# Kernel optimization log

Hardware: AMD Instinct MI355X
Metric: run time of the kernel (lower is better)

## Reference

```python
import jax, jax.numpy as jnp
import numpy as np
from jax.scipy.special import gammaln

N_NODES = 50000
N_EDGES = 1600000
IN_DIM, H1, H2 = 512, 256, 129  # H2 = hid_dims[-1] + 1 (kappa column)


def setup_inputs() -> dict:
    key = jax.random.key(0)
    k1, k2, k3, k4 = jax.random.split(key, 4)
    x = jax.random.normal(k1, (N_NODES, IN_DIM), dtype=jnp.float32)
    edge_index = jax.random.randint(k2, (2, N_EDGES), 0, N_NODES, dtype=jnp.int32)
    # Glorot-ish init for GCN weights
    W0 = jax.random.normal(k3, (IN_DIM, H1), dtype=jnp.float32) * (1.0 / np.sqrt(IN_DIM))
    W1 = jax.random.normal(k4, (H1, H2), dtype=jnp.float32) * (1.0 / np.sqrt(H1))
    return {"x": x, "edge_index": edge_index, "W0": W0, "W1": W1}


def _gcn_conv(h, W, src, dst, norm, n):
    # PyG GCNConv (bias=False): h' = D^-1/2 (A+I) D^-1/2 (h W)
    h = h @ W
    msg = h[src] * norm[:, None]          # [E+N, F_out]
    return jax.ops.segment_sum(msg, dst, num_segments=n)


def reference(x, edge_index, W0, W1):
    n = x.shape[0]
    loops = jnp.arange(n, dtype=edge_index.dtype)
    src = jnp.concatenate([edge_index[0], loops])
    dst = jnp.concatenate([edge_index[1], loops])
    # symmetric normalization with self-loops (deg >= 1, so rsqrt is safe)
    deg = jax.ops.segment_sum(jnp.ones_like(dst, dtype=x.dtype), dst, num_segments=n)
    dinv = jax.lax.rsqrt(deg)
    norm = dinv[src] * dinv[dst]          # [E+N]

    h = jax.nn.softplus(_gcn_conv(x, W0, src, dst, norm, n))
    # dropout is identity in eval mode (training=False)
    h = jax.nn.softplus(_gcn_conv(h, W1, src, dst, norm, n))

    lbd = h[:, :-1]                       # [N, 128] Weibull scale
    kappa = h[:, -1:] + 0.1               # [N, 1]   Weibull shape
    # deterministic (non-random-encoder / eval) reparameterization:
    # z = lbd * exp(lgamma(1 + 1/kappa))  == E[Weibull(lbd, kappa)]
    z = lbd * jnp.exp(gammaln(1.0 + 1.0 / kappa))
    return z, lbd, kappa
```

## Files before the change

kernel.cpp:

```cpp
#include <hip/hip_runtime.h>
#include <hip/hip_bf16.h>
#include <math.h>


typedef unsigned short ushort_t;
typedef __attribute__((ext_vector_type(8))) short bf16x8;
typedef __attribute__((ext_vector_type(4))) float f32x4;

__device__ __forceinline__ ushort_t f2bf(float f) {
    union { float f; unsigned u; } x; x.f = f;
    unsigned r = x.u + 0x7FFF + ((x.u >> 16) & 1);
    return (ushort_t)(r >> 16);
}
__device__ __forceinline__ float bf2f(ushort_t s) {
    union { unsigned u; float f; } x; x.u = ((unsigned)s) << 16; return x.f;
}

__device__ __forceinline__ void async_copy16(const void* gsrc, void* ldst) {
    __builtin_amdgcn_global_load_lds(
        (const __attribute__((address_space(1))) unsigned int*)gsrc,
        (__attribute__((address_space(3))) unsigned int*)ldst,
        16, 0, 0);
}


__global__ __launch_bounds__(256) void count_kernel(const int* __restrict__ dst,
                                                    int* __restrict__ cnt, int E)
{
    int e = blockIdx.x * blockDim.x + threadIdx.x;
    if (e < E) atomicAdd(&cnt[dst[e]], 1);
}

__global__ __launch_bounds__(1024) void scan_local(const int* __restrict__ cnt,
                                                   int* __restrict__ rowptr,
                                                   float* __restrict__ dinv,
                                                   int* __restrict__ blksum, int N)
{
    __shared__ int wsum[16];
    int tid = threadIdx.x, lane = tid & 63, wid = tid >> 6;
    int i = blockIdx.x * 1024 + tid;
    int v = (i < N) ? cnt[i] : 0;
    if (i < N) dinv[i] = rsqrtf((float)(v + 1));
    int s = v;
#pragma unroll
    for (int off = 1; off < 64; off <<= 1) {
        int t = __shfl_up(s, off, 64);
        if (lane >= off) s += t;
    }
    if (lane == 63) wsum[wid] = s;
    __syncthreads();
    if (tid < 16) {
        int w = wsum[tid];
#pragma unroll
        for (int off = 1; off < 16; off <<= 1) {
            int t = __shfl_up(w, off, 64);
            if (tid >= off) w += t;
        }
        wsum[tid] = w;
    }
    __syncthreads();
    int excl = s - v + (wid ? wsum[wid - 1] : 0);
    if (i < N) rowptr[i] = excl;
    if (tid == 0) blksum[blockIdx.x] = wsum[15];
}

__global__ __launch_bounds__(64) void scan_blk(const int* __restrict__ blksum,
                                               int* __restrict__ blkoff,
                                               int nblk, int* __restrict__ rowptr, int N)
{
    int tid = threadIdx.x;
    int v = (tid < nblk) ? blksum[tid] : 0;
    int s = v;
#pragma unroll
    for (int off = 1; off < 64; off <<= 1) {
        int t = __shfl_up(s, off, 64);
        if (tid >= off) s += t;
    }
    if (tid < nblk) blkoff[tid] = s - v;
    if (tid == nblk - 1) rowptr[N] = s;
}

__global__ __launch_bounds__(256) void scan_add(int* __restrict__ rowptr,
                                                int* __restrict__ cursor,
                                                const int* __restrict__ blkoff, int N)
{
    int i = blockIdx.x * blockDim.x + threadIdx.x;
    if (i < N) {
        int r = rowptr[i] + blkoff[i >> 10];
        rowptr[i] = r;
        cursor[i] = r;
    }
}

__global__ __launch_bounds__(256) void scatter_kernel(const int* __restrict__ src,
                                                      const int* __restrict__ dst,
                                                      int* __restrict__ cursor,
                                                      int* __restrict__ col, int E)
{
    int e = blockIdx.x * blockDim.x + threadIdx.x;
    if (e < E) {
        int d = dst[e];
        int pos = atomicAdd(&cursor[d], 1);
        col[pos] = src[e];
    }
}


__global__ __launch_bounds__(256) void conv_x(const float* __restrict__ x,
                                              ushort_t* __restrict__ Abig,
                                              int M, int M_pad)
{
    int id = blockIdx.x * blockDim.x + threadIdx.x;
    int r = id >> 7, q = id & 127;
    if (r >= M_pad) return;
    float4 v = make_float4(0.f, 0.f, 0.f, 0.f);
    if (r < M) v = *reinterpret_cast<const float4*>(&x[(size_t)r * 512 + q * 4]);
    ushort4 h, l;
    h.x = f2bf(v.x); l.x = f2bf(v.x - bf2f(h.x));
    h.y = f2bf(v.y); l.y = f2bf(v.y - bf2f(h.y));
    h.z = f2bf(v.z); l.z = f2bf(v.z - bf2f(h.z));
    h.w = f2bf(v.w); l.w = f2bf(v.w - bf2f(h.w));
    ushort_t* rowp = Abig + (size_t)r * 1024;
    *reinterpret_cast<ushort4*>(rowp + q * 4)       = h;
    *reinterpret_cast<ushort4*>(rowp + 512 + q * 4) = l;
}

__global__ __launch_bounds__(256) void conv_w0(const float* __restrict__ W0,
                                               ushort_t* __restrict__ BT)
{
    int id = blockIdx.x * blockDim.x + threadIdx.x;
    int k = id & 511, n = id >> 9;
    if (n >= 256) return;
    float v = W0[(size_t)k * 256 + n];
    ushort_t h = f2bf(v);
    ushort_t l = f2bf(v - bf2f(h));
    ushort_t* rowp = BT + (size_t)n * 1536;
    rowp[k] = h; rowp[512 + k] = h; rowp[1024 + k] = l;
}

__global__ __launch_bounds__(256) void conv_w1(const float* __restrict__ W1,
                                               ushort_t* __restrict__ BT,
                                               float* __restrict__ W1col)
{
    int id = blockIdx.x * blockDim.x + threadIdx.x;
    int k = id & 255, n = id >> 8;
    if (n >= 128) return;
    float v = W1[(size_t)k * 129 + n];
    ushort_t h = f2bf(v);
    ushort_t l = f2bf(v - bf2f(h));
    ushort_t* rowp = BT + (size_t)n * 768;
    rowp[k] = h; rowp[256 + k] = h; rowp[512 + k] = l;
    if (n == 0) W1col[k] = W1[(size_t)k * 129 + 128];
}

__global__ __launch_bounds__(256) void gemm_bf16(const ushort_t* __restrict__ A, int lda,
                                                 const ushort_t* __restrict__ BT, int ldbt,
                                                 float* __restrict__ C, int ldc,
                                                 int M, int K, int kwrap)
{
    __shared__ short As[128 * 32];
    __shared__ short Bs[128 * 32];

    int tid  = threadIdx.x;
    int w    = tid >> 6;
    int lane = tid & 63;
    int lm   = lane & 15;
    int lq   = lane >> 4;
    int bm   = blockIdx.x * 128;
    int bn   = blockIdx.y * 128;
    int wr   = (w >> 1) * 64;
    int wc   = (w & 1) * 64;

    f32x4 acc[4][4];
#pragma unroll
    for (int i = 0; i < 4; ++i)
#pragma unroll
        for (int j = 0; j < 4; ++j) acc[i][j] = (f32x4)(0.f);

    int srow = (lane >> 2);
    int scol = (lane & 3) * 16;

    for (int k0 = 0; k0 < K; k0 += 32) {
        int ka = (k0 < kwrap) ? k0 : (k0 - kwrap);
#pragma unroll
        for (int q = 0; q < 2; ++q) {
            int r = w * 32 + q * 16 + srow;
            const char* ga = (const char*)A + ((size_t)(bm + r) * lda + ka) * 2 + scol;
            async_copy16(ga, (char*)As + (size_t)(w * 32 + q * 16) * 64);
        }
#pragma unroll
        for (int q = 0; q < 2; ++q) {
            int r = w * 32 + q * 16 + srow;
            const char* gb = (const char*)BT + ((size_t)(bn + r) * ldbt + k0) * 2 + scol;
            async_copy16(gb, (char*)Bs + (size_t)(w * 32 + q * 16) * 64);
        }
        __syncthreads();

        bf16x8 afr[4], bfr[4];
#pragma unroll
        for (int mi = 0; mi < 4; ++mi)
            afr[mi] = *reinterpret_cast<const bf16x8*>(&As[(wr + mi * 16 + lm) * 32 + lq * 8]);
#pragma unroll
        for (int ni = 0; ni < 4; ++ni)
            bfr[ni] = *reinterpret_cast<const bf16x8*>(&Bs[(wc + ni * 16 + lm) * 32 + lq * 8]);
#pragma unroll
        for (int mi = 0; mi < 4; ++mi)
#pragma unroll
            for (int ni = 0; ni < 4; ++ni)
                acc[mi][ni] = __builtin_amdgcn_mfma_f32_16x16x32_bf16(
                    afr[mi], bfr[ni], acc[mi][ni], 0, 0, 0);
        __syncthreads();
    }

#pragma unroll
    for (int mi = 0; mi < 4; ++mi) {
#pragma unroll
        for (int ni = 0; ni < 4; ++ni) {
            int rbase = bm + wr + mi * 16 + lq * 4;
            int cc    = bn + wc + ni * 16 + lm;
#pragma unroll
            for (int e = 0; e < 4; ++e) {
                int r = rbase + e;
                if (r < M) C[(size_t)r * ldc + cc] = acc[mi][ni][e];
            }
        }
    }
}


__device__ __forceinline__ float softplus_f(float x)
{
    return fmaxf(x, 0.f) + log1pf(expf(-fabsf(x)));
}

__device__ __forceinline__ void fma4(float4& a, float w, const float4& v)
{
    a.x = fmaf(w, v.x, a.x);
    a.y = fmaf(w, v.y, a.y);
    a.z = fmaf(w, v.z, a.z);
    a.w = fmaf(w, v.w, a.w);
}

__global__ __launch_bounds__(256) void agg1_kernel(const float* __restrict__ T1,
                                                   const float* __restrict__ dinv,
                                                   const int* __restrict__ rowptr,
                                                   const int* __restrict__ col,
                                                   ushort_t* __restrict__ H1big, int N)
{
    int node = blockIdx.x;
    int tid  = threadIdx.x;
    int c    = tid & 63;
    int slot = tid >> 6;
    float di = dinv[node];
    int beg = rowptr[node], end = rowptr[node + 1];

    float4 acc = make_float4(0.f, 0.f, 0.f, 0.f);
    __shared__ int    s_src[256];
    __shared__ float  s_w[256];
    __shared__ float4 red[4][64];

    for (int base = beg; base < end; base += 256) {
        int cnt = min(256, end - base);
        if (tid < cnt) {
            int s = col[base + tid];
            s_src[tid] = s;
            s_w[tid]   = dinv[s];
        }
        __syncthreads();
        int jb = 0;
        int lim = cnt & ~15;
        for (; jb < lim; jb += 16) {
            int j0 = jb + slot, j1 = j0 + 4, j2 = j0 + 8, j3 = j0 + 12;
            int   s0 = s_src[j0], s1 = s_src[j1], s2 = s_src[j2], s3 = s_src[j3];
            float w0 = s_w[j0],  w1 = s_w[j1],  w2 = s_w[j2],  w3 = s_w[j3];
            float4 v0 = *reinterpret_cast<const float4*>(&T1[(size_t)s0 * 256 + c * 4]);
            float4 v1 = *reinterpret_cast<const float4*>(&T1[(size_t)s1 * 256 + c * 4]);
            float4 v2 = *reinterpret_cast<const float4*>(&T1[(size_t)s2 * 256 + c * 4]);
            float4 v3 = *reinterpret_cast<const float4*>(&T1[(size_t)s3 * 256 + c * 4]);
            fma4(acc, w0, v0); fma4(acc, w1, v1); fma4(acc, w2, v2); fma4(acc, w3, v3);
        }
        for (; jb < cnt; jb += 4) {
            int j = jb + slot;
            if (j < cnt) {
                int   s = s_src[j];
                float w = s_w[j];
                float4 v = *reinterpret_cast<const float4*>(&T1[(size_t)s * 256 + c * 4]);
                fma4(acc, w, v);
            }
        }
        __syncthreads();
    }

    red[slot][c] = acc;
    __syncthreads();
    if (slot == 0) {
        float4 a0 = red[0][c], a1 = red[1][c], a2 = red[2][c], a3 = red[3][c];
        float4 self = *reinterpret_cast<const float4*>(&T1[(size_t)node * 256 + c * 4]);
        float4 o;
        o.x = softplus_f((a0.x + a1.x + a2.x + a3.x + self.x * di) * di);
        o.y = softplus_f((a0.y + a1.y + a2.y + a3.y + self.y * di) * di);
        o.z = softplus_f((a0.z + a1.z + a2.z + a3.z + self.z * di) * di);
        o.w = softplus_f((a0.w + a1.w + a2.w + a3.w + self.w * di) * di);
        ushort4 h, l;
        h.x = f2bf(o.x); l.x = f2bf(o.x - bf2f(h.x));
        h.y = f2bf(o.y); l.y = f2bf(o.y - bf2f(h.y));
        h.z = f2bf(o.z); l.z = f2bf(o.z - bf2f(h.z));
        h.w = f2bf(o.w); l.w = f2bf(o.w - bf2f(h.w));
        ushort_t* rowp = H1big + (size_t)node * 512;
        *reinterpret_cast<ushort4*>(rowp + c * 4)       = h;
        *reinterpret_cast<ushort4*>(rowp + 256 + c * 4) = l;
    }
}

__global__ __launch_bounds__(256) void kappa_col_kernel(const ushort_t* __restrict__ H1big,
                                                        const float* __restrict__ W1col,
                                                        float* __restrict__ T2k, int N)
{
    __shared__ float w[256];
    int tid = threadIdx.x;
    w[tid] = W1col[tid];
    __syncthreads();
    int lane = tid & 63;
    int wid  = tid >> 6;
    int row  = blockIdx.x * 4 + wid;
    if (row >= N) return;
    const ushort_t* rowp = H1big + (size_t)row * 512;
    float s = 0.f;
#pragma unroll
    for (int k = lane; k < 256; k += 64) {
        float hv = bf2f(rowp[k]) + bf2f(rowp[256 + k]);
        s = fmaf(hv, w[k], s);
    }
#pragma unroll
    for (int off = 32; off > 0; off >>= 1)
        s += __shfl_down(s, off, 64);
    if (lane == 0) T2k[row] = s;
}

__global__ __launch_bounds__(256) void agg2_kernel(const float* __restrict__ T2,
                                                   const float* __restrict__ T2k,
                                                   const float* __restrict__ dinv,
                                                   const int* __restrict__ rowptr,
                                                   const int* __restrict__ col,
                                                   float* __restrict__ z_out,
                                                   float* __restrict__ lbd_out,
                                                   float* __restrict__ kap_out, int N)
{
    int node = blockIdx.x;
    int tid  = threadIdx.x;
    int c    = tid & 31;
    int slot = tid >> 5;
    float di = dinv[node];
    int beg = rowptr[node], end = rowptr[node + 1];

    float4 acc  = make_float4(0.f, 0.f, 0.f, 0.f);
    float  acck = 0.f;
    __shared__ int    s_src[256];
    __shared__ float  s_w[256];
    __shared__ float4 red[8][32];
    __shared__ float  s_kred[4];
    __shared__ float  s_g;

    for (int base = beg; base < end; base += 256) {
        int cnt = min(256, end - base);
        if (tid < cnt) {
            int s = col[base + tid];
            float w = dinv[s];
            s_src[tid] = s;
            s_w[tid]   = w;
            acck = fmaf(w, T2k[s], acck);
        }
        __syncthreads();
        int jb = 0;
        int lim = cnt & ~31;
        for (; jb < lim; jb += 32) {
            int j0 = jb + slot, j1 = j0 + 8, j2 = j0 + 16, j3 = j0 + 24;
            int   s0 = s_src[j0], s1 = s_src[j1], s2 = s_src[j2], s3 = s_src[j3];
            float w0 = s_w[j0],  w1 = s_w[j1],  w2 = s_w[j2],  w3 = s_w[j3];
            float4 v0 = *reinterpret_cast<const float4*>(&T2[(size_t)s0 * 128 + c * 4]);
            float4 v1 = *reinterpret_cast<const float4*>(&T2[(size_t)s1 * 128 + c * 4]);
            float4 v2 = *reinterpret_cast<const float4*>(&T2[(size_t)s2 * 128 + c * 4]);
            float4 v3 = *reinterpret_cast<const float4*>(&T2[(size_t)s3 * 128 + c * 4]);
            fma4(acc, w0, v0); fma4(acc, w1, v1); fma4(acc, w2, v2); fma4(acc, w3, v3);
        }
        for (; jb < cnt; jb += 8) {
            int j = jb + slot;
            if (j < cnt) {
                int   s = s_src[j];
                float w = s_w[j];
                float4 v = *reinterpret_cast<const float4*>(&T2[(size_t)s * 128 + c * 4]);
                fma4(acc, w, v);
            }
        }
        __syncthreads();
    }

#pragma unroll
    for (int off = 32; off > 0; off >>= 1)
        acck += __shfl_down(acck, off, 64);
    if ((tid & 63) == 0) s_kred[tid >> 6] = acck;

    red[slot][c] = acc;
    __syncthreads();

    if (tid == 0) {
        float ak = (s_kred[0] + s_kred[1] + s_kred[2] + s_kred[3] + T2k[node] * di) * di;
        float kv = softplus_f(ak) + 0.1f;
        s_g = expf(lgammaf(1.0f + 1.0f / kv));
        kap_out[node] = kv;
    }
    __syncthreads();

    if (slot == 0) {
        float4 a = red[0][c];
#pragma unroll
        for (int p = 1; p < 8; ++p) {
            float4 b = red[p][c];
            a.x += b.x; a.y += b.y; a.z += b.z; a.w += b.w;
        }
        float4 self = *reinterpret_cast<const float4*>(&T2[(size_t)node * 128 + c * 4]);
        float4 sp;
        sp.x = softplus_f((a.x + self.x * di) * di);
        sp.y = softplus_f((a.y + self.y * di) * di);
        sp.z = softplus_f((a.z + self.z * di) * di);
        sp.w = softplus_f((a.w + self.w * di) * di);
        float g = s_g;
        size_t o = (size_t)node * 128 + c * 4;
        *reinterpret_cast<float4*>(&lbd_out[o]) = sp;
        float4 zv = make_float4(sp.x * g, sp.y * g, sp.z * g, sp.w * g);
        *reinterpret_cast<float4*>(&z_out[o]) = zv;
    }
}

extern "C" void kernel_launch(void* const* d_in, const int* in_sizes, int n_in,
                              void* d_out, int out_size, void* d_ws, size_t ws_size,
                              hipStream_t stream)
{
    const float* x  = (const float*)d_in[0];
    const int*   ei = (const int*)d_in[1];
    const float* W0 = (const float*)d_in[2];
    const float* W1 = (const float*)d_in[3];

    const int N = in_sizes[0] / 512;
    const int E = in_sizes[1] / 2;
    const int* src = ei;
    const int* dst = ei + E;

    const int mblocks = (N + 127) / 128;
    const int M_pad   = mblocks * 128;
    const int nchunk  = (N + 1023) / 1024;

    char* w = (char*)d_ws;
    size_t off = 0;
    auto take = [&](size_t bytes) -> void* {
        void* p = (void*)(w + off);
        off = (off + bytes + 255) & ~(size_t)255;
        return p;
    };
    int*      cnt    = (int*)take((size_t)N * 4);
    int*      rowptr = (int*)take((size_t)(N + 1) * 4);
    int*      cursor = (int*)take((size_t)N * 4);
    float*    dinv   = (float*)take((size_t)N * 4);
    int*      col    = (int*)take((size_t)E * 4);
    int*      blksum = (int*)take(64 * 4);
    int*      blkoff = (int*)take(64 * 4);
    ushort_t* W0bigT = (ushort_t*)take((size_t)256 * 1536 * 2);
    ushort_t* W1bigT = (ushort_t*)take((size_t)128 * 768 * 2);
    float*    W1col  = (float*)take((size_t)256 * 4);
    float*    T2k    = (float*)take((size_t)N * 4);
    float*    T1     = (float*)take((size_t)N * 256 * 4);
    float*    T2     = T1;
    ushort_t* Abig   = (ushort_t*)take((size_t)M_pad * 1024 * 2);
    ushort_t* H1big  = Abig;

    float* z_out   = (float*)d_out;
    float* lbd_out = z_out + (size_t)N * 128;
    float* kap_out = lbd_out + (size_t)N * 128;

    hipMemsetAsync(cnt, 0, (size_t)N * 4, stream);
    count_kernel<<<(E + 255) / 256, 256, 0, stream>>>(dst, cnt, E);
    scan_local<<<nchunk, 1024, 0, stream>>>(cnt, rowptr, dinv, blksum, N);
    scan_blk<<<1, 64, 0, stream>>>(blksum, blkoff, nchunk, rowptr, N);
    scan_add<<<(N + 255) / 256, 256, 0, stream>>>(rowptr, cursor, blkoff, N);
    scatter_kernel<<<(E + 255) / 256, 256, 0, stream>>>(src, dst, cursor, col, E);

    conv_x<<<(M_pad * 128) / 256, 256, 0, stream>>>(x, Abig, N, M_pad);
    conv_w0<<<(256 * 512) / 256, 256, 0, stream>>>(W0, W0bigT);
    conv_w1<<<(128 * 256) / 256, 256, 0, stream>>>(W1, W1bigT, W1col);

    dim3 g1(mblocks, 2);
    gemm_bf16<<<g1, 256, 0, stream>>>(Abig, 1024, W0bigT, 1536, T1, 256, N, 1536, 1024);

    agg1_kernel<<<N, 256, 0, stream>>>(T1, dinv, rowptr, col, H1big, N);

    dim3 g2(mblocks, 1);
    gemm_bf16<<<g2, 256, 0, stream>>>(H1big, 512, W1bigT, 768, T2, 128, N, 768, 512);

    kappa_col_kernel<<<(N + 3) / 4, 256, 0, stream>>>(H1big, W1col, T2k, N);
    agg2_kernel<<<N, 256, 0, stream>>>(T2, T2k, dinv, rowptr, col, z_out, lbd_out, kap_out, N);
}
```

Measured before the change: 840.5 us.

## Aggregate one node per wavefront and fuse kappa column into agg1

Both aggregation kernels now assign a single 64-lane wavefront per node, with four nodes per block, instead of a whole 256-thread block per node. This removes the shared-memory staging, __syncthreads barriers and cross-slot reductions. Each lane keeps four independent accumulators so several neighbour loads stay in flight. The kappa-column dot product is fused into agg1 using the fp32 softplus output, which drops the separate kappa_col kernel and its re-read of H1big. The trade-off is less parallelism per node, since each wave walks the neighbour list serially, and agg2 lanes now issue narrower float2 loads.

```diff
diff --git a/kernel.cpp b/kernel.cpp
--- a/kernel.cpp
+++ b/kernel.cpp
@@ -241,100 +241,68 @@
     a.w = fmaf(w, v.w, a.w);
 }
 
+__device__ __forceinline__ void fma2(float2& a, float w, const float2& v)
+{
+    a.x = fmaf(w, v.x, a.x);
+    a.y = fmaf(w, v.y, a.y);
+}
+
 __global__ __launch_bounds__(256) void agg1_kernel(const float* __restrict__ T1,
                                                    const float* __restrict__ dinv,
                                                    const int* __restrict__ rowptr,
                                                    const int* __restrict__ col,
-                                                   ushort_t* __restrict__ H1big, int N)
-{
-    int node = blockIdx.x;
-    int tid  = threadIdx.x;
-    int c    = tid & 63;
-    int slot = tid >> 6;
+                                                   const float* __restrict__ W1col,
+                                                   ushort_t* __restrict__ H1big,
+                                                   float* __restrict__ T2k, int N)
+{
+    int node = blockIdx.x * 4 + (threadIdx.x >> 6);
+    if (node >= N) return;
+    int lane = threadIdx.x & 63;
     float di = dinv[node];
     int beg = rowptr[node], end = rowptr[node + 1];
 
-    float4 acc = make_float4(0.f, 0.f, 0.f, 0.f);
-    __shared__ int    s_src[256];
-    __shared__ float  s_w[256];
-    __shared__ float4 red[4][64];
-
-    for (int base = beg; base < end; base += 256) {
-        int cnt = min(256, end - base);
-        if (tid < cnt) {
-            int s = col[base + tid];
-            s_src[tid] = s;
-            s_w[tid]   = dinv[s];
-        }
-        __syncthreads();
-        int jb = 0;
-        int lim = cnt & ~15;
-        for (; jb < lim; jb += 16) {
-            int j0 = jb + slot, j1 = j0 + 4, j2 = j0 + 8, j3 = j0 + 12;
-            int   s0 = s_src[j0], s1 = s_src[j1], s2 = s_src[j2], s3 = s_src[j3];
-            float w0 = s_w[j0],  w1 = s_w[j1],  w2 = s_w[j2],  w3 = s_w[j3];
-            float4 v0 = *reinterpret_cast<const float4*>(&T1[(size_t)s0 * 256 + c * 4]);
-            float4 v1 = *reinterpret_cast<const float4*>(&T1[(size_t)s1 * 256 + c * 4]);
-            float4 v2 = *reinterpret_cast<const float4*>(&T1[(size_t)s2 * 256 + c * 4]);
-            float4 v3 = *reinterpret_cast<const float4*>(&T1[(size_t)s3 * 256 + c * 4]);
-            fma4(acc, w0, v0); fma4(acc, w1, v1); fma4(acc, w2, v2); fma4(acc, w3, v3);
-        }
-        for (; jb < cnt; jb += 4) {
-            int j = jb + slot;
-            if (j < cnt) {
-                int   s = s_src[j];
-                float w = s_w[j];
-                float4 v = *reinterpret_cast<const float4*>(&T1[(size_t)s * 256 + c * 4]);
-                fma4(acc, w, v);
-            }
-        }
-        __syncthreads();
-    }
-
-    red[slot][c] = acc;
-    __syncthreads();
-    if (slot == 0) {
-        float4 a0 = red[0][c], a1 = red[1][c], a2 = red[2][c], a3 = red[3][c];
-        float4 self = *reinterpret_cast<const float4*>(&T1[(size_t)node * 256 + c * 4]);
-        float4 o;
-        o.x = softplus_f((a0.x + a1.x + a2.x + a3.x + self.x * di) * di);
-        o.y = softplus_f((a0.y + a1.y + a2.y + a3.y + self.y * di) * di);
-        o.z = softplus_f((a0.z + a1.z + a2.z + a3.z + self.z * di) * di);
-        o.w = softplus_f((a0.w + a1.w + a2.w + a3.w + self.w * di) * di);
-        ushort4 h, l;
-        h.x = f2bf(o.x); l.x = f2bf(o.x - bf2f(h.x));
-        h.y = f2bf(o.y); l.y = f2bf(o.y - bf2f(h.y));
-        h.z = f2bf(o.z); l.z = f2bf(o.z - bf2f(h.z));
-        h.w = f2bf(o.w); l.w = f2bf(o.w - bf2f(h.w));
-        ushort_t* rowp = H1big + (size_t)node * 512;
-        *reinterpret_cast<ushort4*>(rowp + c * 4)       = h;
-        *reinterpret_cast<ushort4*>(rowp + 256 + c * 4) = l;
-    }
-}
-
-__global__ __launch_bounds__(256) void kappa_col_kernel(const ushort_t* __restrict__ H1big,
-                                                        const float* __restrict__ W1col,
-                                                        float* __restrict__ T2k, int N)
-{
-    __shared__ float w[256];
-    int tid = threadIdx.x;
-    w[tid] = W1col[tid];
-    __syncthreads();
-    int lane = tid & 63;
-    int wid  = tid >> 6;
-    int row  = blockIdx.x * 4 + wid;
-    if (row >= N) return;
-    const ushort_t* rowp = H1big + (size_t)row * 512;
-    float s = 0.f;
-#pragma unroll
-    for (int k = lane; k < 256; k += 64) {
-        float hv = bf2f(rowp[k]) + bf2f(rowp[256 + k]);
-        s = fmaf(hv, w[k], s);
-    }
+    float4 a0 = make_float4(0.f, 0.f, 0.f, 0.f);
+    float4 a1 = a0, a2 = a0, a3 = a0;
+
+    int e = beg;
+    for (; e + 4 <= end; e += 4) {
+        int s0 = col[e], s1 = col[e + 1], s2 = col[e + 2], s3 = col[e + 3];
+        float w0 = dinv[s0], w1 = dinv[s1], w2 = dinv[s2], w3 = dinv[s3];
+        float4 v0 = *reinterpret_cast<const float4*>(&T1[(size_t)s0 * 256 + lane * 4]);
+        float4 v1 = *reinterpret_cast<const float4*>(&T1[(size_t)s1 * 256 + lane * 4]);
+        float4 v2 = *reinterpret_cast<const float4*>(&T1[(size_t)s2 * 256 + lane * 4]);
+        float4 v3 = *reinterpret_cast<const float4*>(&T1[(size_t)s3 * 256 + lane * 4]);
+        fma4(a0, w0, v0); fma4(a1, w1, v1); fma4(a2, w2, v2); fma4(a3, w3, v3);
+    }
+    for (; e < end; ++e) {
+        int s = col[e];
+        float w = dinv[s];
+        float4 v = *reinterpret_cast<const float4*>(&T1[(size_t)s * 256 + lane * 4]);
+        fma4(a0, w, v);
+    }
+
+    float4 self = *reinterpret_cast<const float4*>(&T1[(size_t)node * 256 + lane * 4]);
+    float4 o;
+    o.x = softplus_f((a0.x + a1.x + a2.x + a3.x + self.x * di) * di);
+    o.y = softplus_f((a0.y + a1.y + a2.y + a3.y + self.y * di) * di);
+    o.z = softplus_f((a0.z + a1.z + a2.z + a3.z + self.z * di) * di);
+    o.w = softplus_f((a0.w + a1.w + a2.w + a3.w + self.w * di) * di);
+
+    ushort4 h, l;
+    h.x = f2bf(o.x); l.x = f2bf(o.x - bf2f(h.x));
+    h.y = f2bf(o.y); l.y = f2bf(o.y - bf2f(h.y));
+    h.z = f2bf(o.z); l.z = f2bf(o.z - bf2f(h.z));
+    h.w = f2bf(o.w); l.w = f2bf(o.w - bf2f(h.w));
+    ushort_t* rowp = H1big + (size_t)node * 512;
+    *reinterpret_cast<ushort4*>(rowp + lane * 4)       = h;
+    *reinterpret_cast<ushort4*>(rowp + 256 + lane * 4) = l;
+
+    float4 wv = *reinterpret_cast<const float4*>(&W1col[lane * 4]);
+    float tk = o.x * wv.x + o.y * wv.y + o.z * wv.z + o.w * wv.w;
 #pragma unroll
     for (int off = 32; off > 0; off >>= 1)
-        s += __shfl_down(s, off, 64);
-    if (lane == 0) T2k[row] = s;
+        tk += __shfl_down(tk, off, 64);
+    if (lane == 0) T2k[node] = tk;
 }
 
 __global__ __launch_bounds__(256) void agg2_kernel(const float* __restrict__ T2,
@@ -346,90 +314,52 @@
                                                    float* __restrict__ lbd_out,
                                                    float* __restrict__ kap_out, int N)
 {
-    int node = blockIdx.x;
-    int tid  = threadIdx.x;
-    int c    = tid & 31;
-    int slot = tid >> 5;
+    int node = blockIdx.x * 4 + (threadIdx.x >> 6);
+    if (node >= N) return;
+    int lane = threadIdx.x & 63;
     float di = dinv[node];
     int beg = rowptr[node], end = rowptr[node + 1];
 
-    float4 acc  = make_float4(0.f, 0.f, 0.f, 0.f);
-    float  acck = 0.f;
-    __shared__ int    s_src[256];
-    __shared__ float  s_w[256];
-    __shared__ float4 red[8][32];
-    __shared__ float  s_kred[4];
-    __shared__ float  s_g;
-
-    for (int base = beg; base < end; base += 256) {
-        int cnt = min(256, end - base);
-        if (tid < cnt) {
-            int s = col[base + tid];
-            float w = dinv[s];
-            s_src[tid] = s;
-            s_w[tid]   = w;
-            acck = fmaf(w, T2k[s], acck);
-        }
-        __syncthreads();
-        int jb = 0;
-        int lim = cnt & ~31;
-        for (; jb < lim; jb += 32) {
-            int j0 = jb + slot, j1 = j0 + 8, j2 = j0 + 16, j3 = j0 + 24;
-            int   s0 = s_src[j0], s1 = s_src[j1], s2 = s_src[j2], s3 = s_src[j3];
-            float w0 = s_w[j0],  w1 = s_w[j1],  w2 = s_w[j2],  w3 = s_w[j3];
-            float4 v0 = *reinterpret_cast<const float4*>(&T2[(size_t)s0 * 128 + c * 4]);
-            float4 v1 = *reinterpret_cast<const float4*>(&T2[(size_t)s1 * 128 + c * 4]);
-            float4 v2 = *reinterpret_cast<const float4*>(&T2[(size_t)s2 * 128 + c * 4]);
-            float4 v3 = *reinterpret_cast<const float4*>(&T2[(size_t)s3 * 128 + c * 4]);
-            fma4(acc, w0, v0); fma4(acc, w1, v1); fma4(acc, w2, v2); fma4(acc, w3, v3);
-        }
-        for (; jb < cnt; jb += 8) {
-            int j = jb + slot;
-            if (j < cnt) {
-                int   s = s_src[j];
-                float w = s_w[j];
-                float4 v = *reinterpret_cast<const float4*>(&T2[(size_t)s * 128 + c * 4]);
-                fma4(acc, w, v);
-            }
-        }
-        __syncthreads();
-    }
-
-#pragma unroll
-    for (int off = 32; off > 0; off >>= 1)
-        acck += __shfl_down(acck, off, 64);
-    if ((tid & 63) == 0) s_kred[tid >> 6] = acck;
-
-    red[slot][c] = acc;
-    __syncthreads();
-
-    if (tid == 0) {
-        float ak = (s_kred[0] + s_kred[1] + s_kred[2] + s_kred[3] + T2k[node] * di) * di;
-        float kv = softplus_f(ak) + 0.1f;
-        s_g = expf(lgammaf(1.0f + 1.0f / kv));
-        kap_out[node] = kv;
-    }
-    __syncthreads();
-
-    if (slot == 0) {
-        float4 a = red[0][c];
-#pragma unroll
-        for (int p = 1; p < 8; ++p) {
-            float4 b = red[p][c];
-            a.x += b.x; a.y += b.y; a.z += b.z; a.w += b.w;
-        }
-        float4 self = *reinterpret_cast<const float4*>(&T2[(size_t)node * 128 + c * 4]);
-        float4 sp;
-        sp.x = softplus_f((a.x + self.x * di) * di);
-        sp.y = softplus_f((a.y + self.y * di) * di);
-        sp.z = softplus_f((a.z + self.z * di) * di);
-        sp.w = softplus_f((a.w + self.w * di) * di);
-        float g = s_g;
-        size_t o = (size_t)node * 128 + c * 4;
-        *reinterpret_cast<float4*>(&lbd_out[o]) = sp;
-        float4 zv = make_float4(sp.x * g, sp.y * g, sp.z * g, sp.w * g);
-        *reinterpret_cast<float4*>(&z_out[o]) = zv;
-    }
+    float2 a0 = make_float2(0.f, 0.f);
+    float2 a1 = a0, a2 = a0, a3 = a0;
+    float k0 = 0.f, k1 = 0.f, k2 = 0.f, k3 = 0.f;
+
+    int e = beg;
+    for (; e + 4 <= end; e += 4) {
+        int s0 = col[e], s1 = col[e + 1], s2 = col[e + 2], s3 = col[e + 3];
+        float w0 = dinv[s0], w1 = dinv[s1], w2 = dinv[s2], w3 = dinv[s3];
+        k0 = fmaf(w0, T2k[s0], k0);
+        k1 = fmaf(w1, T2k[s1], k1);
+        k2 = fmaf(w2, T2k[s2], k2);
+        k3 = fmaf(w3, T2k[s3], k3);
+        float2 v0 = *reinterpret_cast<const float2*>(&T2[(size_t)s0 * 128 + lane * 2]);
+        float2 v1 = *reinterpret_cast<const float2*>(&T2[(size_t)s1 * 128 + lane * 2]);
+        float2 v2 = *reinterpret_cast<const float2*>(&T2[(size_t)s2 * 128 + lane * 2]);
+        float2 v3 = *reinterpret_cast<const float2*>(&T2[(size_t)s3 * 128 + lane * 2]);
+        fma2(a0, w0, v0); fma2(a1, w1, v1); fma2(a2, w2, v2); fma2(a3, w3, v3);
+    }
+    for (; e < end; ++e) {
+        int s = col[e];
+        float w = dinv[s];
+        k0 = fmaf(w, T2k[s], k0);
+        float2 v = *reinterpret_cast<const float2*>(&T2[(size_t)s * 128 + lane * 2]);
+        fma2(a0, w, v);
+    }
+
+    float2 self = *reinterpret_cast<const float2*>(&T2[(size_t)node * 128 + lane * 2]);
+    float2 sp;
+    sp.x = softplus_f((a0.x + a1.x + a2.x + a3.x + self.x * di) * di);
+    sp.y = softplus_f((a0.y + a1.y + a2.y + a3.y + self.y * di) * di);
+
+    float ak = ((k0 + k1 + k2 + k3) + T2k[node] * di) * di;
+    float kv = softplus_f(ak) + 0.1f;
+    float g  = expf(lgammaf(1.0f + 1.0f / kv));
+    if (lane == 0) kap_out[node] = kv;
+
+    size_t o = (size_t)node * 128 + lane * 2;
+    float2 zv = make_float2(sp.x * g, sp.y * g);
+    *reinterpret_cast<float2*>(&lbd_out[o]) = sp;
+    *reinterpret_cast<float2*>(&z_out[o])   = zv;
 }
 
 extern "C" void kernel_launch(void* const* d_in, const int* in_sizes, int n_in,
@@ -491,11 +421,11 @@
     dim3 g1(mblocks, 2);
     gemm_bf16<<<g1, 256, 0, stream>>>(Abig, 1024, W0bigT, 1536, T1, 256, N, 1536, 1024);
 
-    agg1_kernel<<<N, 256, 0, stream>>>(T1, dinv, rowptr, col, H1big, N);
+    agg1_kernel<<<(N + 3) / 4, 256, 0, stream>>>(T1, dinv, rowptr, col, W1col, H1big, T2k, N);
 
     dim3 g2(mblocks, 1);
     gemm_bf16<<<g2, 256, 0, stream>>>(H1big, 512, W1bigT, 768, T2, 128, N, 768, 512);
 
-    kappa_col_kernel<<<(N + 3) / 4, 256, 0, stream>>>(H1big, W1col, T2k, N);
-    agg2_kernel<<<N, 256, 0, stream>>>(T2, T2k, dinv, rowptr, col, z_out, lbd_out, kap_out, N);
-}
+    agg2_kernel<<<(N + 3) / 4, 256, 0, stream>>>(T2, T2k, dinv, rowptr, col,
+                                                 z_out, lbd_out, kap_out, N);
+}
```

Result: faster. 820.6 us (-2.4%).
